# Kernel tuning notes

Hardware: AMD Instinct MI355X
Metric: run time of the kernel (lower is better)

Reference implementation:

```python
import jax, jax.numpy as jnp
import numpy as np

T, B, C, HF, H, W, E, TOP_K = 4, 32, 384, 1536, 14, 14, 8, 2
AUX_W = 0.01
ALPHA = 2.0  # spikingjelly ATan surrogate default

@jax.custom_vjp
def spike(v):
    return (v >= 0.0).astype(v.dtype)

def _spike_fwd(v):
    return spike(v), v

def _spike_bwd(v, g):
    sg = (ALPHA / 2.0) / (1.0 + (jnp.pi / 2.0 * ALPHA * v) ** 2)
    return (g * sg,)

spike.defvjp(_spike_fwd, _spike_bwd)

def lif_multistep(x, tau):
    # x: (T, ...). decay_input=True, v_threshold=1, hard reset to 0, detach_reset
    def step(v, xt):
        v = v + (xt - v) / tau
        s = spike(v - 1.0)
        v = v * (1.0 - jax.lax.stop_gradient(s))
        return v, s
    _, s = jax.lax.scan(step, jnp.zeros_like(x[0]), x)
    return s

def bn_eval(y, gamma, beta, mean, var, eps=1e-5):
    inv = gamma / jnp.sqrt(var + eps)
    return y * inv[None, :, None, None] + (beta - mean * inv)[None, :, None, None]

def setup_inputs() -> dict:
    key = jax.random.key(0)
    ks = jax.random.split(key, 8)
    d = {"x": jax.random.normal(ks[0], (T, B, C, H, W), jnp.float32)}
    d["rw"] = jax.random.normal(ks[1], (E, C), jnp.float32) * 0.02
    d["rb"] = jnp.zeros((E,), jnp.float32)
    d["r_gamma"] = jnp.ones((E,), jnp.float32)
    d["r_beta"] = jnp.zeros((E,), jnp.float32)
    d["r_mean"] = jax.random.normal(ks[2], (E,), jnp.float32) * 0.01
    d["r_var"] = jax.random.uniform(ks[3], (E,), jnp.float32, 0.75, 1.25)
    d["w1"] = jax.random.normal(ks[4], (E, HF, C), jnp.float32) * 0.02
    d["b1"] = jnp.zeros((E, HF), jnp.float32)
    d["g1"] = jnp.ones((E, HF), jnp.float32)
    d["be1"] = jnp.zeros((E, HF), jnp.float32)
    d["m1"] = jax.random.normal(ks[5], (E, HF), jnp.float32) * 0.01
    d["v1"] = jnp.ones((E, HF), jnp.float32)
    d["w2"] = jax.random.normal(ks[6], (E, C, HF), jnp.float32) * 0.02
    d["b2"] = jnp.zeros((E, C), jnp.float32)
    d["g2"] = jnp.ones((E, C), jnp.float32)
    d["be2"] = jnp.zeros((E, C), jnp.float32)
    d["m2"] = jax.random.normal(ks[7], (E, C), jnp.float32) * 0.01
    d["v2"] = jnp.ones((E, C), jnp.float32)
    d["taus"] = jnp.linspace(1.5, 4.0, E, dtype=jnp.float32)
    return d

def reference(x, rw, rb, r_gamma, r_beta, r_mean, r_var,
              w1, b1, g1, be1, m1, v1, w2, b2, g2, be2, m2, v2, taus):
    Tn, Bn, Cn, Hn, Wn = x.shape
    N = Tn * Bn
    # ---- SpikeRouter ----
    s = lif_multistep(x, 2.0)                                   # (T,B,C,H,W)
    r = jnp.einsum('tbchw,ec->tbehw', s, rw) + rb[None, None, :, None, None]
    r = bn_eval(r.reshape(N, E, Hn, Wn), r_gamma, r_beta, r_mean, r_var)
    logits = r.mean(axis=(-2, -1))                              # (N,E)
    probs = jax.nn.softmax(logits, axis=-1)
    tkw, tki = jax.lax.top_k(probs, TOP_K)
    tkw = tkw / tkw.sum(axis=-1, keepdims=True)
    one_hot = jax.nn.one_hot(tki, E, dtype=x.dtype)             # (N,K,E)
    gate = (one_hot * tkw[..., None]).sum(axis=1)               # (N,E), 0 for unselected
    # ---- expert dispatch/combine (dense, math-equivalent: gate==0 masks out) ----
    xt = x.reshape(N, Cn, Hn, Wn)
    out = jnp.zeros_like(xt)
    for e in range(E):
        s1 = spike(xt / taus[e] - 1.0)                          # T=1 LIF step
        h = jnp.einsum('nchw,oc->nohw', s1, w1[e]) + b1[e][None, :, None, None]
        h = bn_eval(h, g1[e], be1[e], m1[e], v1[e])
        s2 = spike(h / taus[e] - 1.0)
        o = jnp.einsum('nchw,oc->nohw', s2, w2[e]) + b2[e][None, :, None, None]
        o = bn_eval(o, g2[e], be2[e], m2[e], v2[e])
        o = o + xt                                              # final residual
        out = out + gate[:, e, None, None, None] * o
    # ---- Switch-style load balancing loss ----
    f = one_hot.sum(axis=1).mean(axis=0)                        # fraction routed per expert
    p = probs.mean(axis=0)
    aux = AUX_W * E * jnp.sum(f * p)
    return out.reshape(Tn, Bn, Cn, Hn, Wn), aux
```

## Files before the change

### kernel.cpp

```cpp
#include <hip/hip_runtime.h>
#include <hip/hip_bf16.h>
#include <cstdint>
#include <math.h>

#define T_  4
#define B_  32
#define C_  384
#define HF_ 1536
#define HW_ 196
#define E_  8
#define N_  128
#define REC_CAP 16384
#define NROW 1792
#define NGT  50176
#define LCAP 64

#define LIFB (B_ * C_)
#define TRB  (E_ * 12 * 24)
#define PRB  48

__global__ __launch_bounds__(256) void k_lifprep(
    const float* __restrict__ x, float* __restrict__ cnt,
    const float* __restrict__ w1, __hip_bfloat16* __restrict__ w1t,
    const float* b1, const float* g1, const float* be1,
    const float* m1, const float* v1,
    const float* b2, const float* g2, const float* be2,
    const float* m2, const float* v2,
    const float* taus,
    float* A, float* Bc, float* const2, float* inv2v,
    float* rowmaxp, int* header) {
  __shared__ float tile[64][33];
  __shared__ int c4[T_];
  int blk = blockIdx.x;
  int tid = threadIdx.x;

  if (blk < LIFB) {
    if (tid < T_) c4[tid] = 0;
    __syncthreads();
    int bc = blk;
    bool act = tid < HW_;
    float v = 0.f;
    size_t base = (size_t)bc * HW_ + (act ? tid : 0);
    #pragma unroll
    for (int t = 0; t < T_; ++t) {
      float xv = act ? x[base + (size_t)t * B_ * C_ * HW_] : -1e30f;
      v = v + (xv - v) * 0.5f;
      bool sp = (v - 1.0f >= 0.0f);
      if (sp) v = 0.f;
      unsigned long long m = __ballot(act && sp);
      if ((tid & 63) == 0) atomicAdd(&c4[t], __popcll(m));
    }
    __syncthreads();
    if (tid < T_) cnt[(size_t)tid * B_ * C_ + bc] = (float)c4[tid];
  } else if (blk < LIFB + TRB) {
    int rem = blk - LIFB;
    int e = rem / 288, r2 = rem % 288;
    int ct = r2 / 24, ot = r2 % 24;
    int c0 = ct * 32, o0 = ot * 64;
    int cl = tid & 31, olb = tid >> 5;
    #pragma unroll
    for (int it = 0; it < 8; ++it) {
      int ol = olb + it * 8;
      tile[ol][cl] = w1[(size_t)(e * HF_ + o0 + ol) * C_ + c0 + cl];
    }
    __syncthreads();
    int ol2 = tid & 63, clb = tid >> 6;
    #pragma unroll
    for (int it = 0; it < 8; ++it) {
      int cl2 = clb + it * 4;
      w1t[(size_t)(e * C_ + c0 + cl2) * HF_ + o0 + ol2] =
          __float2bfloat16(tile[ol2][cl2]);
    }
    if (tid < 32) {
      float m = 0.f;
      for (int ol = 0; ol < 64; ++ol) {
        float bv = __bfloat162float(__float2bfloat16(tile[ol][tid]));
        m = fmaxf(m, fabsf(bv));
      }
      rowmaxp[(size_t)(e * C_ + c0 + tid) * 24 + ot] = m;
    }
  } else {
    int idx = (blk - LIFB - TRB) * 256 + tid;
    if (idx < 64) header[idx] = 0;
    if (idx < E_ * HF_) {
      int e = idx / HF_;
      float inv = g1[idx] / sqrtf(v1[idx] + 1e-5f);
      float sh  = be1[idx] - m1[idx] * inv;
      A[idx]  = inv;
      Bc[idx] = inv * b1[idx] + sh - taus[e];
    }
    if (idx < E_ * C_) {
      float inv = g2[idx] / sqrtf(v2[idx] + 1e-5f);
      const2[idx] = b2[idx] * inv + (be2[idx] - m2[idx] * inv);
      inv2v[idx]  = inv;
    }
  }
}

__global__ __launch_bounds__(256) void k_router(
    const float* __restrict__ cnt, const float* __restrict__ rw,
    const float* rb, const float* rg, const float* rbeta,
    const float* rmean, const float* rvar,
    const float* __restrict__ const2,
    const float* __restrict__ rowmaxp, float* __restrict__ rowmax,
    const float* __restrict__ A, const float* __restrict__ Bc,
    float* __restrict__ thrmin,
    int* sel_e, float* sel_g, float* gsum, float* K,
    float* f_acc, float* p_acc) {
  __shared__ float sc[C_ + 256 + E_];
  __shared__ int s_i1, s_i2;
  __shared__ float s_g1, s_g2;
  int bid = blockIdx.x, tid = threadIdx.x;

  if (bid < N_) {
    int n = bid;
    float* part = sc + C_;
    float* lg = part + 256;
    for (int c = tid; c < C_; c += 256) sc[c] = cnt[(size_t)n * C_ + c];
    __syncthreads();
    {
      int e = tid >> 5, sub = tid & 31;
      float d = 0.f;
      for (int c = sub; c < C_; c += 32) d += rw[e * C_ + c] * sc[c];
      part[tid] = d;
    }
    __syncthreads();
    if (tid < E_) {
      float dot = 0.f;
      #pragma unroll
      for (int j = 0; j < 32; ++j) dot += part[tid * 32 + j];
      float inv = rg[tid] / sqrtf(rvar[tid] + 1e-5f);
      lg[tid] = (dot * (1.0f / HW_) + rb[tid]) * inv +
                (rbeta[tid] - rmean[tid] * inv);
    }
    __syncthreads();
    if (tid == 0) {
      float m = lg[0];
      for (int e = 1; e < E_; ++e) m = fmaxf(m, lg[e]);
      float pr[E_]; float s = 0.f;
      for (int e = 0; e < E_; ++e) { pr[e] = expf(lg[e] - m); s += pr[e]; }
      float invs = 1.0f / s;
      for (int e = 0; e < E_; ++e) pr[e] *= invs;
      int i1 = 0;
      for (int e = 1; e < E_; ++e) if (pr[e] > pr[i1]) i1 = e;
      int i2 = (i1 == 0) ? 1 : 0;
      for (int e = 0; e < E_; ++e) if (e != i1 && pr[e] > pr[i2]) i2 = e;
      float w = pr[i1] + pr[i2];
      float ga = pr[i1] / w, gb = pr[i2] / w;
      sel_e[2 * n] = i1; sel_e[2 * n + 1] = i2;
      sel_g[2 * n] = ga; sel_g[2 * n + 1] = gb;
      gsum[n] = ga + gb;
      s_i1 = i1; s_i2 = i2; s_g1 = ga; s_g2 = gb;
      atomicAdd(&f_acc[i1], 1.0f);
      atomicAdd(&f_acc[i2], 1.0f);
      for (int e = 0; e < E_; ++e) atomicAdd(&p_acc[e], pr[e]);
    }
    __syncthreads();
    int i1 = s_i1, i2 = s_i2; float ga = s_g1, gb = s_g2;
    for (int c = tid; c < C_; c += 256)
      K[(size_t)n * C_ + c] =
          ga * const2[i1 * C_ + c] + gb * const2[i2 * C_ + c];
  } else if (bid < N_ + 12) {
    int idx = (bid - N_) * 256 + tid;
    if (idx < E_ * C_) {
      float m = 0.f;
      #pragma unroll
      for (int t = 0; t < 24; ++t) m = fmaxf(m, rowmaxp[(size_t)idx * 24 + t]);
      rowmax[idx] = m;
    }
  } else {
    float* red = sc;
    for (int e = 0; e < E_; ++e) {
      float m = INFINITY;
      for (int o = tid; o < HF_; o += 256) {
        float a = A[e * HF_ + o], b = Bc[e * HF_ + o];
        float thr = (a != 0.0f) ? (-b / fabsf(a))
                                : ((b >= 0.0f) ? -INFINITY : INFINITY);
        m = fminf(m, thr);
      }
      red[tid] = m;
      __syncthreads();
      for (int s = 128; s > 0; s >>= 1) {
        if (tid < s) red[tid] = fminf(red[tid], red[tid + s]);
        __syncthreads();
      }
      if (tid == 0) thrmin[e] = red[0];
      __syncthreads();
    }
  }
}

__global__ __launch_bounds__(256) void k_lists(
    const float* __restrict__ x, const int* __restrict__ sel_e,
    const float* __restrict__ taus, const float* __restrict__ rowmax,
    const float* __restrict__ thrmin,
    unsigned short* __restrict__ list16,
    int* __restrict__ queue, int* __restrict__ qcount) {
  __shared__ float xs[14 * 385];
  int bid = blockIdx.x, tid = threadIdx.x;
  int lane = tid & 63, wave = tid >> 6;
  int n = bid / 14, h = bid - n * 14;
  unsigned long long lmask = (1ull << lane) - 1ull;

  for (int idx = tid; idx < C_ * 7; idx += 256) {
    int c = idx / 7, wp = idx - c * 7;
    float2 v = *(const float2*)(x + ((size_t)(n * C_ + c) * 14 + h) * 14 + 2 * wp);
    xs[(2 * wp) * 385 + c]     = v.x;
    xs[(2 * wp + 1) * 385 + c] = v.y;
  }
  __syncthreads();

  for (int t = wave; t < 28; t += 4) {
    int k = t / 14, w = t - k * 14;
    int pair = 2 * n + k;
    int e = sel_e[pair];
    float tau = taus[e];
    const float* rme = rowmax + e * C_;
    unsigned long long masks[6];
    int nnz = 0;
    float myb = 0.f;
    #pragma unroll
    for (int cb = 0; cb < 6; ++cb) {
      int c = cb * 64 + lane;
      bool sp = (xs[w * 385 + c] / tau - 1.0f >= 0.0f);
      unsigned long long m = __ballot(sp);
      masks[cb] = m;
      if (sp) myb += rme[c];
      nnz += __popcll(m);
    }
    #pragma unroll
    for (int off = 1; off < 64; off <<= 1) myb += __shfl_xor(myb, off, 64);
    bool prune = (myb < thrmin[e] - 1e-4f);
    if (!prune) {
      int tw = pair * 196 + h * 14 + w;
      size_t lbase = (size_t)tw * LCAP;
      int cum = 0;
      #pragma unroll
      for (int cb = 0; cb < 6; ++cb) {
        unsigned long long m = masks[cb];
        bool sp = (m >> lane) & 1ull;
        int pos = cum + __popcll(m & lmask);
        if (sp && pos < LCAP) list16[lbase + pos] = (unsigned short)(cb * 64 + lane);
        cum += __popcll(m);
      }
      if (lane == 0) {
        int nv = nnz < LCAP ? nnz : LCAP;
        int qi = atomicAdd(qcount, 1);
        queue[qi] = tw | (nv << 20);
      }
    }
  }
}

__global__ __launch_bounds__(256) void k_combine(
    const float* __restrict__ x, const float* __restrict__ gsum,
    const float* __restrict__ K, float* __restrict__ out) {
  int idx = blockIdx.x * 256 + threadIdx.x;
  int nc = idx / 49;
  float g = gsum[nc / C_];
  float kc = K[nc];
  float4 v = ((const float4*)x)[idx];
  v.x = g * v.x + kc;
  v.y = g * v.y + kc;
  v.z = g * v.z + kc;
  v.w = g * v.w + kc;
  ((float4*)out)[idx] = v;
}

__global__ __launch_bounds__(256, 4) void k_gather(
    const __hip_bfloat16* __restrict__ w1t,
    const float* __restrict__ A, const float* __restrict__ Bc,
    const int* __restrict__ sel_e,
    const int* __restrict__ queue, const int* __restrict__ qcount,
    const unsigned short* __restrict__ list16,
    int* __restrict__ rec, int* __restrict__ rec_count) {
  int nq = *qcount;
  int wid = blockIdx.x * 4 + (threadIdx.x >> 6);
  int lane = threadIdx.x & 63;
  int nwaves = gridDim.x * 4;

  for (int qi = wid; qi < nq; qi += nwaves) {
    int ent = queue[qi];
    int tw = ent & 0xFFFFF;
    int nnz = ent >> 20;
    int pair = tw / 196, pos = tw - pair * 196;
    int e = sel_e[pair];
    int lv = (int)list16[(size_t)tw * LCAP + lane];
    const uint4* wb = (const uint4*)(w1t + (size_t)e * C_ * HF_);

    #pragma unroll
    for (int pass = 0; pass < 3; ++pass) {
      const uint4* wbp = wb + pass * 64 + lane;
      float acc[8];
      #pragma unroll
      for (int q = 0; q < 8; ++q) acc[q] = 0.f;
      int j = 0;
      for (; j + 4 <= nnz; j += 4) {
        int c0 = __shfl(lv, j + 0);
        int c1 = __shfl(lv, j + 1);
        int c2 = __shfl(lv, j + 2);
        int c3 = __shfl(lv, j + 3);
        uint4 a = wbp[c0 * 192];
        uint4 b = wbp[c1 * 192];
        uint4 c = wbp[c2 * 192];
        uint4 d = wbp[c3 * 192];
        uint32_t ua[4] = {a.x, a.y, a.z, a.w};
        uint32_t ub[4] = {b.x, b.y, b.z, b.w};
        uint32_t uc[4] = {c.x, c.y, c.z, c.w};
        uint32_t ud[4] = {d.x, d.y, d.z, d.w};
        #pragma unroll
        for (int q = 0; q < 4; ++q) {
          acc[2 * q]     += __uint_as_float(ua[q] << 16) + __uint_as_float(ub[q] << 16) +
                            __uint_as_float(uc[q] << 16) + __uint_as_float(ud[q] << 16);
          acc[2 * q + 1] += __uint_as_float(ua[q] & 0xffff0000u) + __uint_as_float(ub[q] & 0xffff0000u) +
                            __uint_as_float(uc[q] & 0xffff0000u) + __uint_as_float(ud[q] & 0xffff0000u);
        }
      }
      for (; j < nnz; ++j) {
        int c0 = __shfl(lv, j);
        uint4 a = wbp[c0 * 192];
        uint32_t ua[4] = {a.x, a.y, a.z, a.w};
        #pragma unroll
        for (int q = 0; q < 4; ++q) {
          acc[2 * q]     += __uint_as_float(ua[q] << 16);
          acc[2 * q + 1] += __uint_as_float(ua[q] & 0xffff0000u);
        }
      }
      int k2 = (pass * 64 + lane) * 2;
      float4 Av0 = ((const float4*)(A + e * HF_))[k2];
      float4 Av1 = ((const float4*)(A + e * HF_))[k2 + 1];
      float4 Bv0 = ((const float4*)(Bc + e * HF_))[k2];
      float4 Bv1 = ((const float4*)(Bc + e * HF_))[k2 + 1];
      float av[8] = {Av0.x, Av0.y, Av0.z, Av0.w, Av1.x, Av1.y, Av1.z, Av1.w};
      float bv[8] = {Bv0.x, Bv0.y, Bv0.z, Bv0.w, Bv1.x, Bv1.y, Bv1.z, Bv1.w};
      #pragma unroll
      for (int q = 0; q < 8; ++q) {
        if (av[q] * acc[q] + bv[q] >= 0.0f) {
          int ridx = atomicAdd(rec_count, 1);
          if (ridx < REC_CAP) {
            rec[ridx * 3 + 0] = pair;
            rec[ridx * 3 + 1] = pos;
            rec[ridx * 3 + 2] = (pass * 64 + lane) * 8 + q;
          }
        }
      }
    }
  }
}

__global__ void k_apply(const int* __restrict__ rec, const int* __restrict__ rec_count,
                        const int* __restrict__ sel_e, const float* __restrict__ sel_g,
                        const float* __restrict__ inv2v, const float* __restrict__ w2,
                        const float* f_acc, const float* p_acc,
                        float* __restrict__ out, float* aux_out) {
  int nrec = *rec_count;
  if (nrec > REC_CAP) nrec = REC_CAP;
  for (int r = blockIdx.x; r < nrec; r += gridDim.x) {
    int pair = rec[r * 3], pos = rec[r * 3 + 1], o = rec[r * 3 + 2];
    int n = pair >> 1;
    int e = sel_e[pair];
    float g = sel_g[pair];
    for (int c = threadIdx.x; c < C_; c += blockDim.x) {
      float wv = w2[(size_t)(e * C_ + c) * HF_ + o];
      atomicAdd(&out[(size_t)(n * C_ + c) * HW_ + pos],
                g * inv2v[e * C_ + c] * wv);
    }
  }
  if (blockIdx.x == 0 && threadIdx.x == 0) {
    float s = 0.f;
    for (int e = 0; e < E_; ++e)
      s += (f_acc[e] * (1.0f / N_)) * (p_acc[e] * (1.0f / N_));
    *aux_out = 0.01f * E_ * s;
  }
}

extern "C" void kernel_launch(void* const* d_in, const int* in_sizes, int n_in,
                              void* d_out, int out_size, void* d_ws, size_t ws_size,
                              hipStream_t stream) {
  const float* x       = (const float*)d_in[0];
  const float* rw      = (const float*)d_in[1];
  const float* rb      = (const float*)d_in[2];
  const float* r_gamma = (const float*)d_in[3];
  const float* r_beta  = (const float*)d_in[4];
  const float* r_mean  = (const float*)d_in[5];
  const float* r_var   = (const float*)d_in[6];
  const float* w1      = (const float*)d_in[7];
  const float* b1      = (const float*)d_in[8];
  const float* g1      = (const float*)d_in[9];
  const float* be1     = (const float*)d_in[10];
  const float* m1      = (const float*)d_in[11];
  const float* v1      = (const float*)d_in[12];
  const float* w2      = (const float*)d_in[13];
  const float* b2      = (const float*)d_in[14];
  const float* g2      = (const float*)d_in[15];
  const float* be2     = (const float*)d_in[16];
  const float* m2      = (const float*)d_in[17];
  const float* v2      = (const float*)d_in[18];
  const float* taus    = (const float*)d_in[19];
  float* out = (float*)d_out;

  char* ws = (char*)d_ws;
  int*   header = (int*)ws;
  float* f_acc  = (float*)ws + 8;
  float* p_acc  = (float*)ws + 16;
  float* cnt    = (float*)(ws + 256);
  int*   sel_e  = (int*)(ws + 196864);
  float* sel_g  = (float*)(ws + 197888);
  float* gsum   = (float*)(ws + 198912);
  float* K      = (float*)(ws + 199424);
  float* A      = (float*)(ws + 396032);
  float* Bc     = (float*)(ws + 445184);
  float* const2 = (float*)(ws + 494336);
  float* inv2v  = (float*)(ws + 506624);
  int*   rec    = (int*)(ws + 518912);
  __hip_bfloat16* w1t = (__hip_bfloat16*)(ws + 715520);
  int*   queue  = (int*)(ws + 10152704);
  unsigned short* list16 = (unsigned short*)(ws + 10353408);
  float* rowmaxp = (float*)(ws + 16775936);
  float* rowmax  = (float*)(ws + 17070848);
  float* thrmin  = (float*)(ws + 17083136);
  int* qcount = header + 1;

  k_lifprep<<<LIFB + TRB + PRB, 256, 0, stream>>>(
      x, cnt, w1, w1t, b1, g1, be1, m1, v1, b2, g2, be2, m2, v2, taus,
      A, Bc, const2, inv2v, rowmaxp, header);
  k_router<<<N_ + 13, 256, 0, stream>>>(
      cnt, rw, rb, r_gamma, r_beta, r_mean, r_var, const2,
      rowmaxp, rowmax, A, Bc, thrmin,
      sel_e, sel_g, gsum, K, f_acc, p_acc);
  k_lists<<<NROW, 256, 0, stream>>>(
      x, sel_e, taus, rowmax, thrmin, list16, queue, qcount);
  k_combine<<<(N_ * C_ * 49) / 256, 256, 0, stream>>>(x, gsum, K, out);
  k_gather<<<2048, 256, 0, stream>>>(
      w1t, A, Bc, sel_e, queue, qcount, list16, rec, header);
  k_apply<<<64, 256, 0, stream>>>(
      rec, header, sel_e, sel_g, inv2v, w2, f_acc, p_acc,
      out, out + (out_size - 1));
}
```

Measured before the change: 219.9 us.

## Precompute per-expert spike levels as bytes and bucket gather queues by expert

```diff
diff --git a/kernel.cpp b/kernel.cpp
--- a/kernel.cpp
+++ b/kernel.cpp
@@ -11,7 +11,7 @@
 #define E_  8
 #define N_  128
 #define REC_CAP 16384
-#define NROW 1792
+#define NPAIR 256
 #define NGT  50176
 #define LCAP 64
 
@@ -21,6 +21,7 @@
 
 __global__ __launch_bounds__(256) void k_lifprep(
     const float* __restrict__ x, float* __restrict__ cnt,
+    unsigned char* __restrict__ levels,
     const float* __restrict__ w1, __hip_bfloat16* __restrict__ w1t,
     const float* b1, const float* g1, const float* be1,
     const float* m1, const float* v1,
@@ -37,6 +38,18 @@
   if (blk < LIFB) {
     if (tid < T_) c4[tid] = 0;
     __syncthreads();
+    float te[E_];
+    #pragma unroll
+    for (int e2 = 0; e2 < E_; ++e2) {
+      float t = taus[e2];
+      float y = t;
+      #pragma unroll
+      for (int it = 0; it < 4; ++it) {
+        float cnd = __uint_as_float(__float_as_uint(y) - 1u);
+        if (cnd / t - 1.0f >= 0.0f) y = cnd; else break;
+      }
+      te[e2] = y;
+    }
     int bc = blk;
     bool act = tid < HW_;
     float v = 0.f;
@@ -49,6 +62,12 @@
       if (sp) v = 0.f;
       unsigned long long m = __ballot(act && sp);
       if ((tid & 63) == 0) atomicAdd(&c4[t], __popcll(m));
+      if (act) {
+        int lvl = 0;
+        #pragma unroll
+        for (int e2 = 0; e2 < E_; ++e2) lvl += (xv >= te[e2]) ? 1 : 0;
+        levels[(size_t)t * B_ * C_ * HW_ + base] = (unsigned char)lvl;
+      }
     }
     __syncthreads();
     if (tid < T_) cnt[(size_t)tid * B_ * C_ + bc] = (float)c4[tid];
@@ -191,62 +210,58 @@
 }
 
 __global__ __launch_bounds__(256) void k_lists(
-    const float* __restrict__ x, const int* __restrict__ sel_e,
-    const float* __restrict__ taus, const float* __restrict__ rowmax,
-    const float* __restrict__ thrmin,
+    const unsigned char* __restrict__ levels, const int* __restrict__ sel_e,
+    const float* __restrict__ rowmax, const float* __restrict__ thrmin,
     unsigned short* __restrict__ list16,
     int* __restrict__ queue, int* __restrict__ qcount) {
-  __shared__ float xs[14 * 385];
+  __shared__ unsigned char xs8[C_ * HW_];
+  __shared__ float rmx[C_];
   int bid = blockIdx.x, tid = threadIdx.x;
   int lane = tid & 63, wave = tid >> 6;
-  int n = bid / 14, h = bid - n * 14;
+  int pair = bid, n = bid >> 1;
+  int e = sel_e[pair];
   unsigned long long lmask = (1ull << lane) - 1ull;
 
-  for (int idx = tid; idx < C_ * 7; idx += 256) {
-    int c = idx / 7, wp = idx - c * 7;
-    float2 v = *(const float2*)(x + ((size_t)(n * C_ + c) * 14 + h) * 14 + 2 * wp);
-    xs[(2 * wp) * 385 + c]     = v.x;
-    xs[(2 * wp + 1) * 385 + c] = v.y;
-  }
+  {
+    const uint4* src = (const uint4*)(levels + (size_t)n * (C_ * HW_));
+    uint4* dst = (uint4*)xs8;
+    for (int i = tid; i < (C_ * HW_) / 16; i += 256) dst[i] = src[i];
+  }
+  for (int c = tid; c < C_; c += 256) rmx[c] = rowmax[e * C_ + c];
   __syncthreads();
 
-  for (int t = wave; t < 28; t += 4) {
-    int k = t / 14, w = t - k * 14;
-    int pair = 2 * n + k;
-    int e = sel_e[pair];
-    float tau = taus[e];
-    const float* rme = rowmax + e * C_;
+  float thr = thrmin[e] - 1e-4f;
+  for (int pos = wave; pos < HW_; pos += 4) {
     unsigned long long masks[6];
     int nnz = 0;
     float myb = 0.f;
     #pragma unroll
     for (int cb = 0; cb < 6; ++cb) {
       int c = cb * 64 + lane;
-      bool sp = (xs[w * 385 + c] / tau - 1.0f >= 0.0f);
+      bool sp = (int)xs8[c * HW_ + pos] > e;
       unsigned long long m = __ballot(sp);
       masks[cb] = m;
-      if (sp) myb += rme[c];
+      if (sp) myb += rmx[c];
       nnz += __popcll(m);
     }
     #pragma unroll
     for (int off = 1; off < 64; off <<= 1) myb += __shfl_xor(myb, off, 64);
-    bool prune = (myb < thrmin[e] - 1e-4f);
-    if (!prune) {
-      int tw = pair * 196 + h * 14 + w;
+    if (myb >= thr) {
+      int tw = pair * HW_ + pos;
       size_t lbase = (size_t)tw * LCAP;
       int cum = 0;
       #pragma unroll
       for (int cb = 0; cb < 6; ++cb) {
         unsigned long long m = masks[cb];
-        bool sp = (m >> lane) & 1ull;
-        int pos = cum + __popcll(m & lmask);
-        if (sp && pos < LCAP) list16[lbase + pos] = (unsigned short)(cb * 64 + lane);
+        bool sp2 = (m >> lane) & 1ull;
+        int p2 = cum + __popcll(m & lmask);
+        if (sp2 && p2 < LCAP) list16[lbase + p2] = (unsigned short)(cb * 64 + lane);
         cum += __popcll(m);
       }
       if (lane == 0) {
         int nv = nnz < LCAP ? nnz : LCAP;
-        int qi = atomicAdd(qcount, 1);
-        queue[qi] = tw | (nv << 20);
+        int qi = atomicAdd(&qcount[e], 1);
+        queue[e * NGT + qi] = tw | (nv << 20);
       }
     }
   }
@@ -270,77 +285,78 @@
 __global__ __launch_bounds__(256, 4) void k_gather(
     const __hip_bfloat16* __restrict__ w1t,
     const float* __restrict__ A, const float* __restrict__ Bc,
-    const int* __restrict__ sel_e,
     const int* __restrict__ queue, const int* __restrict__ qcount,
     const unsigned short* __restrict__ list16,
     int* __restrict__ rec, int* __restrict__ rec_count) {
-  int nq = *qcount;
   int wid = blockIdx.x * 4 + (threadIdx.x >> 6);
   int lane = threadIdx.x & 63;
   int nwaves = gridDim.x * 4;
 
-  for (int qi = wid; qi < nq; qi += nwaves) {
-    int ent = queue[qi];
-    int tw = ent & 0xFFFFF;
-    int nnz = ent >> 20;
-    int pair = tw / 196, pos = tw - pair * 196;
-    int e = sel_e[pair];
-    int lv = (int)list16[(size_t)tw * LCAP + lane];
+  for (int e = 0; e < E_; ++e) {
+    int nq = qcount[e];
+    const int* qe = queue + e * NGT;
     const uint4* wb = (const uint4*)(w1t + (size_t)e * C_ * HF_);
-
-    #pragma unroll
-    for (int pass = 0; pass < 3; ++pass) {
-      const uint4* wbp = wb + pass * 64 + lane;
-      float acc[8];
+    for (int qi = wid; qi < nq; qi += nwaves) {
+      int ent = qe[qi];
+      int tw = ent & 0xFFFFF;
+      int nnz = ent >> 20;
+      int pair = tw / HW_, pos = tw - pair * HW_;
+      int lv = (int)list16[(size_t)tw * LCAP + lane];
+
       #pragma unroll
-      for (int q = 0; q < 8; ++q) acc[q] = 0.f;
-      int j = 0;
-      for (; j + 4 <= nnz; j += 4) {
-        int c0 = __shfl(lv, j + 0);
-        int c1 = __shfl(lv, j + 1);
-        int c2 = __shfl(lv, j + 2);
-        int c3 = __shfl(lv, j + 3);
-        uint4 a = wbp[c0 * 192];
-        uint4 b = wbp[c1 * 192];
-        uint4 c = wbp[c2 * 192];
-        uint4 d = wbp[c3 * 192];
-        uint32_t ua[4] = {a.x, a.y, a.z, a.w};
-        uint32_t ub[4] = {b.x, b.y, b.z, b.w};
-        uint32_t uc[4] = {c.x, c.y, c.z, c.w};
-        uint32_t ud[4] = {d.x, d.y, d.z, d.w};
+      for (int pass = 0; pass < 3; ++pass) {
+        const uint4* wbp = wb + pass * 64 + lane;
+        float acc[8];
         #pragma unroll
-        for (int q = 0; q < 4; ++q) {
-          acc[2 * q]     += __uint_as_float(ua[q] << 16) + __uint_as_float(ub[q] << 16) +
-                            __uint_as_float(uc[q] << 16) + __uint_as_float(ud[q] << 16);
-          acc[2 * q + 1] += __uint_as_float(ua[q] & 0xffff0000u) + __uint_as_float(ub[q] & 0xffff0000u) +
-                            __uint_as_float(uc[q] & 0xffff0000u) + __uint_as_float(ud[q] & 0xffff0000u);
+        for (int q = 0; q < 8; ++q) acc[q] = 0.f;
+        int j = 0;
+        for (; j + 4 <= nnz; j += 4) {
+          int c0 = __shfl(lv, j + 0);
+          int c1 = __shfl(lv, j + 1);
+          int c2 = __shfl(lv, j + 2);
+          int c3 = __shfl(lv, j + 3);
+          uint4 a = wbp[c0 * 192];
+          uint4 b = wbp[c1 * 192];
+          uint4 c = wbp[c2 * 192];
+          uint4 d = wbp[c3 * 192];
+          uint32_t ua[4] = {a.x, a.y, a.z, a.w};
+          uint32_t ub[4] = {b.x, b.y, b.z, b.w};
+          uint32_t uc[4] = {c.x, c.y, c.z, c.w};
+          uint32_t ud[4] = {d.x, d.y, d.z, d.w};
+          #pragma unroll
+          for (int q = 0; q < 4; ++q) {
+            acc[2 * q]     += __uint_as_float(ua[q] << 16) + __uint_as_float(ub[q] << 16) +
+                              __uint_as_float(uc[q] << 16) + __uint_as_float(ud[q] << 16);
+            acc[2 * q + 1] += __uint_as_float(ua[q] & 0xffff0000u) + __uint_as_float(ub[q] & 0xffff0000u) +
+                              __uint_as_float(uc[q] & 0xffff0000u) + __uint_as_float(ud[q] & 0xffff0000u);
+          }
         }
-      }
-      for (; j < nnz; ++j) {
-        int c0 = __shfl(lv, j);
-        uint4 a = wbp[c0 * 192];
-        uint32_t ua[4] = {a.x, a.y, a.z, a.w};
+        for (; j < nnz; ++j) {
+          int c0 = __shfl(lv, j);
+          uint4 a = wbp[c0 * 192];
+          uint32_t ua[4] = {a.x, a.y, a.z, a.w};
+          #pragma unroll
+          for (int q = 0; q < 4; ++q) {
+            acc[2 * q]     += __uint_as_float(ua[q] << 16);
+            acc[2 * q + 1] += __uint_as_float(ua[q] & 0xffff0000u);
+          }
+        }
+        int k2 = (pass * 64 + lane) * 2;
+        float4 Av0 = ((const float4*)(A + e * HF_))[k2];
+        float4 Av1 = ((const float4*)(A + e * HF_))[k2 + 1];
+        float4 Bv0 = ((const float4*)(Bc + e * HF_))[k2];
+        float4 Bv1 = ((const float4*)(Bc + e * HF_))[k2 + 1];
+        float av[8] = {Av0.x, Av0.y, Av0.z, Av0.w, Av1.x, Av1.y, Av1.z, Av1.w};
+        float bv[8] = {Bv0.x, Bv0.y, Bv0.z, Bv0.w, Bv1.x, Bv1.y, Bv1.z, Bv1.w};
         #pragma unroll
-        for (int q = 0; q < 4; ++q) {
-          acc[2 * q]     += __uint_as_float(ua[q] << 16);
-          acc[2 * q + 1] += __uint_as_float(ua[q] & 0xffff0000u);
-        }
-      }
-      int k2 = (pass * 64 + lane) * 2;
-      float4 Av0 = ((const float4*)(A + e * HF_))[k2];
-      float4 Av1 = ((const float4*)(A + e * HF_))[k2 + 1];
-      float4 Bv0 = ((const float4*)(Bc + e * HF_))[k2];
-      float4 Bv1 = ((const float4*)(Bc + e * HF_))[k2 + 1];
-      float av[8] = {Av0.x, Av0.y, Av0.z, Av0.w, Av1.x, Av1.y, Av1.z, Av1.w};
-      float bv[8] = {Bv0.x, Bv0.y, Bv0.z, Bv0.w, Bv1.x, Bv1.y, Bv1.z, Bv1.w};
-      #pragma unroll
-      for (int q = 0; q < 8; ++q) {
-        if (av[q] * acc[q] + bv[q] >= 0.0f) {
-          int ridx = atomicAdd(rec_count, 1);
-          if (ridx < REC_CAP) {
-            rec[ridx * 3 + 0] = pair;
-            rec[ridx * 3 + 1] = pos;
-            rec[ridx * 3 + 2] = (pass * 64 + lane) * 8 + q;
+        for (int q = 0; q < 8; ++q) {
+          if (av[q] * acc[q] + bv[q] >= 0.0f) {
+            int ridx = atomicAdd(rec_count, 1);
+            if (ridx < REC_CAP) {
+              rec[ridx * 3 + 0] = pair;
+              rec[ridx * 3 + 1] = pos;
+              rec[ridx * 3 + 2] = (pass * 64 + lane) * 8 + q;
+            }
           }
         }
       }
@@ -403,6 +419,7 @@
   int*   header = (int*)ws;
   float* f_acc  = (float*)ws + 8;
   float* p_acc  = (float*)ws + 16;
+  int*   qcount = header + 32;
   float* cnt    = (float*)(ws + 256);
   int*   sel_e  = (int*)(ws + 196864);
   float* sel_g  = (float*)(ws + 197888);
@@ -415,24 +432,24 @@
   int*   rec    = (int*)(ws + 518912);
   __hip_bfloat16* w1t = (__hip_bfloat16*)(ws + 715520);
   int*   queue  = (int*)(ws + 10152704);
-  unsigned short* list16 = (unsigned short*)(ws + 10353408);
-  float* rowmaxp = (float*)(ws + 16775936);
-  float* rowmax  = (float*)(ws + 17070848);
-  float* thrmin  = (float*)(ws + 17083136);
-  int* qcount = header + 1;
+  unsigned short* list16 = (unsigned short*)(ws + 11758336);
+  unsigned char* levels  = (unsigned char*)(ws + 18180864);
+  float* rowmaxp = (float*)(ws + 27814656);
+  float* rowmax  = (float*)(ws + 28109568);
+  float* thrmin  = (float*)(ws + 28121856);
 
   k_lifprep<<<LIFB + TRB + PRB, 256, 0, stream>>>(
-      x, cnt, w1, w1t, b1, g1, be1, m1, v1, b2, g2, be2, m2, v2, taus,
+      x, cnt, levels, w1, w1t, b1, g1, be1, m1, v1, b2, g2, be2, m2, v2, taus,
       A, Bc, const2, inv2v, rowmaxp, header);
   k_router<<<N_ + 13, 256, 0, stream>>>(
       cnt, rw, rb, r_gamma, r_beta, r_mean, r_var, const2,
       rowmaxp, rowmax, A, Bc, thrmin,
       sel_e, sel_g, gsum, K, f_acc, p_acc);
-  k_lists<<<NROW, 256, 0, stream>>>(
-      x, sel_e, taus, rowmax, thrmin, list16, queue, qcount);
+  k_lists<<<NPAIR, 256, 0, stream>>>(
+      levels, sel_e, rowmax, thrmin, list16, queue, qcount);
   k_combine<<<(N_ * C_ * 49) / 256, 256, 0, stream>>>(x, gsum, K, out);
   k_gather<<<2048, 256, 0, stream>>>(
-      w1t, A, Bc, sel_e, queue, qcount, list16, rec, header);
+      w1t, A, Bc, queue, qcount, list16, rec, header);
   k_apply<<<64, 256, 0, stream>>>(
       rec, header, sel_e, sel_g, inv2v, w2, f_acc, p_acc,
       out, out + (out_size - 1));
```

Result: slower. 269.8 us (+22.7%).

## Fuse sparse second-layer apply into gather kernel via wave ballot

Applied to the files above, without the earlier changes.

```diff
diff --git a/kernel.cpp b/kernel.cpp
--- a/kernel.cpp
+++ b/kernel.cpp
@@ -10,7 +10,6 @@
 #define HW_ 196
 #define E_  8
 #define N_  128
-#define REC_CAP 16384
 #define NROW 1792
 #define NGT  50176
 #define LCAP 64
@@ -195,12 +194,21 @@
     const float* __restrict__ taus, const float* __restrict__ rowmax,
     const float* __restrict__ thrmin,
     unsigned short* __restrict__ list16,
-    int* __restrict__ queue, int* __restrict__ qcount) {
+    int* __restrict__ queue, int* __restrict__ qcount,
+    const float* __restrict__ f_acc, const float* __restrict__ p_acc,
+    float* __restrict__ aux_out) {
   __shared__ float xs[14 * 385];
   int bid = blockIdx.x, tid = threadIdx.x;
   int lane = tid & 63, wave = tid >> 6;
   int n = bid / 14, h = bid - n * 14;
   unsigned long long lmask = (1ull << lane) - 1ull;
+
+  if (bid == 0 && tid == 0) {
+    float s = 0.f;
+    for (int e = 0; e < E_; ++e)
+      s += (f_acc[e] * (1.0f / N_)) * (p_acc[e] * (1.0f / N_));
+    *aux_out = 0.01f * E_ * s;
+  }
 
   for (int idx = tid; idx < C_ * 7; idx += 256) {
     int c = idx / 7, wp = idx - c * 7;
@@ -270,10 +278,11 @@
 __global__ __launch_bounds__(256, 4) void k_gather(
     const __hip_bfloat16* __restrict__ w1t,
     const float* __restrict__ A, const float* __restrict__ Bc,
-    const int* __restrict__ sel_e,
+    const int* __restrict__ sel_e, const float* __restrict__ sel_g,
     const int* __restrict__ queue, const int* __restrict__ qcount,
     const unsigned short* __restrict__ list16,
-    int* __restrict__ rec, int* __restrict__ rec_count) {
+    const float* __restrict__ inv2v, const float* __restrict__ w2,
+    float* __restrict__ out) {
   int nq = *qcount;
   int wid = blockIdx.x * 4 + (threadIdx.x >> 6);
   int lane = threadIdx.x & 63;
@@ -283,7 +292,8 @@
     int ent = queue[qi];
     int tw = ent & 0xFFFFF;
     int nnz = ent >> 20;
-    int pair = tw / 196, pos = tw - pair * 196;
+    int pair = tw / HW_, pos = tw - pair * HW_;
+    int n = pair >> 1;
     int e = sel_e[pair];
     int lv = (int)list16[(size_t)tw * LCAP + lane];
     const uint4* wb = (const uint4*)(w1t + (size_t)e * C_ * HF_);
@@ -335,42 +345,21 @@
       float bv[8] = {Bv0.x, Bv0.y, Bv0.z, Bv0.w, Bv1.x, Bv1.y, Bv1.z, Bv1.w};
       #pragma unroll
       for (int q = 0; q < 8; ++q) {
-        if (av[q] * acc[q] + bv[q] >= 0.0f) {
-          int ridx = atomicAdd(rec_count, 1);
-          if (ridx < REC_CAP) {
-            rec[ridx * 3 + 0] = pair;
-            rec[ridx * 3 + 1] = pos;
-            rec[ridx * 3 + 2] = (pass * 64 + lane) * 8 + q;
+        unsigned long long fm = __ballot(av[q] * acc[q] + bv[q] >= 0.0f);
+        while (fm) {
+          int b = __ffsll((unsigned long long)fm) - 1;
+          fm &= fm - 1;
+          int o = (pass * 64 + b) * 8 + q;
+          float gk = sel_g[pair];
+          const float* w2r = w2 + (size_t)e * C_ * HF_ + o;
+          const float* ivr = inv2v + e * C_;
+          for (int c = lane; c < C_; c += 64) {
+            atomicAdd(&out[((size_t)(n * C_ + c)) * HW_ + pos],
+                      gk * ivr[c] * w2r[(size_t)c * HF_]);
           }
         }
       }
     }
-  }
-}
-
-__global__ void k_apply(const int* __restrict__ rec, const int* __restrict__ rec_count,
-                        const int* __restrict__ sel_e, const float* __restrict__ sel_g,
-                        const float* __restrict__ inv2v, const float* __restrict__ w2,
-                        const float* f_acc, const float* p_acc,
-                        float* __restrict__ out, float* aux_out) {
-  int nrec = *rec_count;
-  if (nrec > REC_CAP) nrec = REC_CAP;
-  for (int r = blockIdx.x; r < nrec; r += gridDim.x) {
-    int pair = rec[r * 3], pos = rec[r * 3 + 1], o = rec[r * 3 + 2];
-    int n = pair >> 1;
-    int e = sel_e[pair];
-    float g = sel_g[pair];
-    for (int c = threadIdx.x; c < C_; c += blockDim.x) {
-      float wv = w2[(size_t)(e * C_ + c) * HF_ + o];
-      atomicAdd(&out[(size_t)(n * C_ + c) * HW_ + pos],
-                g * inv2v[e * C_ + c] * wv);
-    }
-  }
-  if (blockIdx.x == 0 && threadIdx.x == 0) {
-    float s = 0.f;
-    for (int e = 0; e < E_; ++e)
-      s += (f_acc[e] * (1.0f / N_)) * (p_acc[e] * (1.0f / N_));
-    *aux_out = 0.01f * E_ * s;
   }
 }
 
@@ -412,7 +401,6 @@
   float* Bc     = (float*)(ws + 445184);
   float* const2 = (float*)(ws + 494336);
   float* inv2v  = (float*)(ws + 506624);
-  int*   rec    = (int*)(ws + 518912);
   __hip_bfloat16* w1t = (__hip_bfloat16*)(ws + 715520);
   int*   queue  = (int*)(ws + 10152704);
   unsigned short* list16 = (unsigned short*)(ws + 10353408);
@@ -429,11 +417,9 @@
       rowmaxp, rowmax, A, Bc, thrmin,
       sel_e, sel_g, gsum, K, f_acc, p_acc);
   k_lists<<<NROW, 256, 0, stream>>>(
-      x, sel_e, taus, rowmax, thrmin, list16, queue, qcount);
+      x, sel_e, taus, rowmax, thrmin, list16, queue, qcount,
+      f_acc, p_acc, out + (out_size - 1));
   k_combine<<<(N_ * C_ * 49) / 256, 256, 0, stream>>>(x, gsum, K, out);
   k_gather<<<2048, 256, 0, stream>>>(
-      w1t, A, Bc, sel_e, queue, qcount, list16, rec, header);
-  k_apply<<<64, 256, 0, stream>>>(
-      rec, header, sel_e, sel_g, inv2v, w2, f_acc, p_acc,
-      out, out + (out_size - 1));
-}
+      w1t, A, Bc, sel_e, sel_g, queue, qcount, list16, inv2v, w2, out);
+}
```

New measurement: 221.1 us. Within noise of the previous version (+0.5%).
